# Optimization experiments

Hardware: AMD Instinct MI355X
Metric: run time of the kernel (lower is better)

Reference implementation:

```python
import jax, jax.numpy as jnp
import numpy as np

N_NODES = 8192
N_EDGES = 131072

_DIMS = [
    ("cnn1", 3, 32), ("cnn2", 32, 64), ("cnn3", 64, 128),
    ("gcn1", 128, 256), ("gcn2", 256, 512), ("gcn3", 512, 1024),
    ("cnnd1", 1024, 512), ("cnnd2", 512, 256), ("cnnd3", 256, 128), ("cnnd4", 128, 50),
]


def setup_inputs() -> dict:
    key = jax.random.key(0)
    ks = jax.random.split(key, 2 + 2 * len(_DIMS))
    inp = {
        "x": jax.random.normal(ks[0], (N_NODES, 3), dtype=jnp.float32),
        "edge_index": jax.random.randint(ks[1], (2, N_EDGES), 0, N_NODES, dtype=jnp.int64)
        if jax.config.jax_enable_x64 else
        jax.random.randint(ks[1], (2, N_EDGES), 0, N_NODES, dtype=jnp.int32),
    }
    for i, (name, din, dout) in enumerate(_DIMS):
        scale = 1.0 / np.sqrt(din)
        inp[name + "_w"] = jax.random.normal(ks[2 + 2 * i], (din, dout), dtype=jnp.float32) * scale
        inp[name + "_b"] = jax.random.normal(ks[3 + 2 * i], (dout,), dtype=jnp.float32) * scale
    return inp


def _gcn_norm(edge_index, n, dtype):
    # add self-loops, symmetric normalization D^{-1/2}(A+I)D^{-1/2}
    loop = jnp.arange(n, dtype=edge_index.dtype)
    src = jnp.concatenate([edge_index[0], loop])
    dst = jnp.concatenate([edge_index[1], loop])
    deg = jax.ops.segment_sum(jnp.ones_like(dst, dtype=dtype), dst, num_segments=n)
    dinv = jnp.where(deg > 0, 1.0 / jnp.sqrt(deg), 0.0)
    norm = dinv[src] * dinv[dst]  # [E+N]
    return src, dst, norm


def _forward(x, edge_index,
             cnn1_w, cnn1_b, cnn2_w, cnn2_b, cnn3_w, cnn3_b,
             gcn1_w, gcn1_b, gcn2_w, gcn2_b, gcn3_w, gcn3_b,
             cnnd1_w, cnnd1_b, cnnd2_w, cnnd2_b, cnnd3_w, cnnd3_b, cnnd4_w, cnnd4_b):
    n = x.shape[0]
    src, dst, norm = _gcn_norm(edge_index, n, x.dtype)

    def lin(h, w, b):  # 1x1 Conv1d == per-node linear
        return h @ w + b

    def gcn(h, w, b):
        hl = h @ w                                    # [N, out]
        msg = hl[src] * norm[:, None]                 # gather + scale [E+N, out]
        return jax.ops.segment_sum(msg, dst, num_segments=n) + b

    h = jax.nn.relu(lin(x, cnn1_w, cnn1_b))
    h = jax.nn.relu(lin(h, cnn2_w, cnn2_b))
    h = jax.nn.relu(lin(h, cnn3_w, cnn3_b))
    h = jax.nn.relu(gcn(h, gcn1_w, gcn1_b))
    h = jax.nn.relu(gcn(h, gcn2_w, gcn2_b))
    h = jax.nn.relu(gcn(h, gcn3_w, gcn3_b))
    h = jax.nn.relu(lin(h, cnnd1_w, cnnd1_b))
    h = jax.nn.relu(lin(h, cnnd2_w, cnnd2_b))
    h = jax.nn.relu(lin(h, cnnd3_w, cnnd3_b))
    h = lin(h, cnnd4_w, cnnd4_b)
    return jax.nn.softmax(h, axis=1)  # [N, output_dim]


def reference(x, edge_index,
              cnn1_w, cnn1_b, cnn2_w, cnn2_b, cnn3_w, cnn3_b,
              gcn1_w, gcn1_b, gcn2_w, gcn2_b, gcn3_w, gcn3_b,
              cnnd1_w, cnnd1_b, cnnd2_w, cnnd2_b, cnnd3_w, cnnd3_b, cnnd4_w, cnnd4_b):
    return _forward(x, edge_index,
                    cnn1_w, cnn1_b, cnn2_w, cnn2_b, cnn3_w, cnn3_b,
                    gcn1_w, gcn1_b, gcn2_w, gcn2_b, gcn3_w, gcn3_b,
                    cnnd1_w, cnnd1_b, cnnd2_w, cnnd2_b, cnnd3_w, cnnd3_b, cnnd4_w, cnnd4_b)
```

## Files before the change

### kernel.cpp

```cpp
#include <hip/hip_runtime.h>
#include <math.h>

#define N_NODES 8192
#define N_EDGES 131072

typedef unsigned short u16;
typedef unsigned int u32;
typedef short bf16x8 __attribute__((ext_vector_type(8)));
typedef int v4i __attribute__((ext_vector_type(4)));
typedef float f32x4 __attribute__((ext_vector_type(4)));

__device__ __forceinline__ u16 f2bf(float x) {
    unsigned u = __float_as_uint(x);
    u += 0x7fffu + ((u >> 16) & 1u);
    return (u16)(u >> 16);
}
__device__ __forceinline__ float bf2f(u16 h) { return __uint_as_float(((unsigned)h) << 16); }

#define GLD_LDS(gp, lp) __builtin_amdgcn_global_load_lds( \
    (const __attribute__((address_space(1))) void*)(gp),  \
    (__attribute__((address_space(3))) void*)(lp), 16, 0, 0)

template <int N> __device__ __forceinline__ void wait_vmcnt() {
    if constexpr (N == 0) asm volatile("s_waitcnt vmcnt(0)" ::: "memory");
    else if constexpr (N == 4) asm volatile("s_waitcnt vmcnt(4)" ::: "memory");
    else if constexpr (N == 8) asm volatile("s_waitcnt vmcnt(8)" ::: "memory");
    else static_assert(N < 0, "unsupported vmcnt");
}

__device__ __forceinline__ u32 lds_addr(const void* p) {
    return (u32)(size_t)(const __attribute__((address_space(3))) void*)p;
}

__device__ __forceinline__ bf16x8 lds_read_b128(u32 addr) {
    v4i r;
    asm volatile("ds_read_b128 %0, %1" : "=v"(r) : "v"(addr));
    union { v4i i; bf16x8 b; } u;
    u.i = r;
    return u.b;
}

template <int NU> struct UV;
template <> struct UV<1> { typedef u32 T; };
template <> struct UV<2> { typedef uint2 T; };
template <> struct UV<4> { typedef uint4 T; };


__global__ void k_zero_deg(int* __restrict__ deg) {
    int i = blockIdx.x * 256 + threadIdx.x;
    if (i < N_NODES) deg[i] = 0;
}

__global__ void k_count(const int* __restrict__ ei, int* __restrict__ deg) {
    int e = blockIdx.x * 256 + threadIdx.x;
    if (e < N_EDGES) atomicAdd(&deg[ei[N_EDGES + e]], 1);
}

__global__ __launch_bounds__(1024) void k_scan(const int* __restrict__ deg,
                                               int* __restrict__ rowptr,
                                               int* __restrict__ pos,
                                               float* __restrict__ dinv) {
    __shared__ int sums[1024];
    int t = threadIdx.x;
    int local[8];
    int s = 0;
#pragma unroll
    for (int i = 0; i < 8; ++i) {
        local[i] = deg[t * 8 + i];
        dinv[t * 8 + i] = 1.0f / sqrtf((float)(local[i] + 1));
        s += local[i];
    }
    sums[t] = s;
    __syncthreads();
    for (int off = 1; off < 1024; off <<= 1) {
        int v = (t >= off) ? sums[t - off] : 0;
        __syncthreads();
        sums[t] += v;
        __syncthreads();
    }
    int run = sums[t] - s;
#pragma unroll
    for (int i = 0; i < 8; ++i) {
        rowptr[t * 8 + i] = run;
        pos[t * 8 + i] = run;
        run += local[i];
    }
    if (t == 1023) rowptr[8192] = run;
}

__global__ void k_fill(const int* __restrict__ ei, const float* __restrict__ dinv,
                       int* __restrict__ pos, int* __restrict__ csr_src,
                       float* __restrict__ csr_w) {
    int e = blockIdx.x * 256 + threadIdx.x;
    if (e < N_EDGES) {
        int s = ei[e];
        int t = ei[N_EDGES + e];
        int idx = atomicAdd(&pos[t], 1);
        csr_src[idx] = s;
        csr_w[idx] = dinv[s] * dinv[t];
    }
}

__global__ void k_prep_all(const float* __restrict__ g1w, const float* __restrict__ g2w,
                           const float* __restrict__ g3w, const float* __restrict__ d1w,
                           const float* __restrict__ d2w, const float* __restrict__ d3w,
                           u16* __restrict__ wts) {
    int idx = blockIdx.x * 256 + threadIdx.x;
    const float* W;
    int local, lgK, N;
    u16 *hi, *lo;
    if (idx < 32768)        { W = g1w; local = idx;           lgK = 7;  N = 256;  hi = wts;           lo = wts + 32768; }
    else if (idx < 163840)  { W = g2w; local = idx - 32768;   lgK = 8;  N = 512;  hi = wts + 65536;   lo = wts + 196608; }
    else if (idx < 688128)  { W = g3w; local = idx - 163840;  lgK = 9;  N = 1024; hi = wts + 327680;  lo = wts + 851968; }
    else if (idx < 1212416) { W = d1w; local = idx - 688128;  lgK = 10; N = 512;  hi = wts + 1376256; lo = wts + 1900544; }
    else if (idx < 1343488) { W = d2w; local = idx - 1212416; lgK = 9;  N = 256;  hi = wts + 2424832; lo = wts + 2555904; }
    else if (idx < 1376256) { W = d3w; local = idx - 1343488; lgK = 8;  N = 128;  hi = wts + 2686976; lo = wts + 2719744; }
    else return;
    int n = local >> lgK;
    int k = local & ((1 << lgK) - 1);
    float v = W[(size_t)k * N + n];
    u16 h = f2bf(v);
    int dst = ((k >> 3) * N + n) * 8 + (k & 7);
    hi[dst] = h;
    lo[dst] = f2bf(v - bf2f(h));
}

__global__ __launch_bounds__(256) void k_enc_fused(const float* __restrict__ x,
                                                   const float* __restrict__ w1, const float* __restrict__ b1,
                                                   const float* __restrict__ w2, const float* __restrict__ b2,
                                                   const float* __restrict__ w3, const float* __restrict__ b3,
                                                   u16* __restrict__ Chi, u16* __restrict__ Clo) {
    __shared__ float lw[10560];
    const int tid = threadIdx.x;
    for (int i = tid; i < 96; i += 256) lw[i] = w1[i];
    for (int i = tid; i < 32; i += 256) lw[96 + i] = b1[i];
    for (int i = tid; i < 2048; i += 256) lw[128 + i] = w2[i];
    for (int i = tid; i < 64; i += 256) lw[2176 + i] = b2[i];
    for (int i = tid; i < 8192; i += 256) lw[2240 + i] = w3[i];
    for (int i = tid; i < 128; i += 256) lw[10432 + i] = b3[i];
    __syncthreads();

    const int lane = tid & 63;
    const int node = blockIdx.x * 4 + (tid >> 6);

    float x0 = x[node * 3 + 0], x1 = x[node * 3 + 1], x2 = x[node * 3 + 2];

    int o1 = lane & 31;
    float h1 = fmaxf(x0 * lw[o1] + x1 * lw[32 + o1] + x2 * lw[64 + o1] + lw[96 + o1], 0.f);

    float h2 = lw[2176 + lane];
#pragma unroll
    for (int k = 0; k < 32; ++k) h2 += __shfl(h1, k) * lw[128 + k * 64 + lane];
    h2 = fmaxf(h2, 0.f);

    float h3a = lw[10432 + lane];
    float h3b = lw[10432 + 64 + lane];
#pragma unroll
    for (int k = 0; k < 64; ++k) {
        float hk = __shfl(h2, k);
        h3a += hk * lw[2240 + k * 128 + lane];
        h3b += hk * lw[2240 + k * 128 + 64 + lane];
    }
    h3a = fmaxf(h3a, 0.f);
    h3b = fmaxf(h3b, 0.f);

    size_t base = (size_t)node * 128;
    u16 ha = f2bf(h3a), hb = f2bf(h3b);
    Chi[base + lane] = ha;
    Chi[base + 64 + lane] = hb;
    Clo[base + lane] = f2bf(h3a - bf2f(ha));
    Clo[base + 64 + lane] = f2bf(h3b - bf2f(hb));
}

__global__ __launch_bounds__(256) void k_d4sm_fused(const float* __restrict__ A,
                                                    const float* __restrict__ W,
                                                    const float* __restrict__ bias,
                                                    float* __restrict__ out) {
    __shared__ float lw[6450];
    const int tid = threadIdx.x;
    for (int i = tid; i < 6400; i += 256) lw[i] = W[i];
    for (int i = tid; i < 50; i += 256) lw[6400 + i] = bias[i];
    __syncthreads();

    const int lane = tid & 63;
    const int node = blockIdx.x * 4 + (tid >> 6);

    float a0 = A[(size_t)node * 128 + lane];
    float a1 = A[(size_t)node * 128 + 64 + lane];

    float acc = (lane < 50) ? lw[6400 + lane] : 0.f;
    int oc = (lane < 50) ? lane : 0;
#pragma unroll
    for (int k = 0; k < 64; ++k) acc += __shfl(a0, k) * lw[k * 50 + oc];
#pragma unroll
    for (int k = 0; k < 64; ++k) acc += __shfl(a1, k) * lw[(64 + k) * 50 + oc];

    float v = (lane < 50) ? acc : -INFINITY;
    float m = v;
#pragma unroll
    for (int off = 32; off; off >>= 1) m = fmaxf(m, __shfl_xor(m, off));
    float e = (lane < 50) ? expf(v - m) : 0.f;
    float s = e;
#pragma unroll
    for (int off = 32; off; off >>= 1) s += __shfl_xor(s, off);
    if (lane < 50) out[(size_t)node * 50 + lane] = e / s;
}

template <int D>
__global__ __launch_bounds__(256) void k_agg_s(const u16* __restrict__ hi_in,
                                               const u16* __restrict__ lo_in,
                                               u16* __restrict__ hi_out,
                                               u16* __restrict__ lo_out,
                                               const int* __restrict__ rowptr,
                                               const int* __restrict__ csr_src,
                                               const float* __restrict__ csr_w,
                                               const float* __restrict__ dinv) {
    constexpr int EPL = D / 64;
    constexpr int NU = EPL / 2;
    using VT = typename UV<NU>::T;
    int node = blockIdx.x * 4 + (threadIdx.x >> 6);
    int lane = threadIdx.x & 63;
    const size_t off = (size_t)node * D + lane * EPL;
    float acc[EPL];
    {
        float dn = dinv[node];
        float w0 = dn * dn;
        u32 hu[NU], lu[NU];
        *(VT*)hu = *(const VT*)(hi_in + off);
        *(VT*)lu = *(const VT*)(lo_in + off);
#pragma unroll
        for (int j = 0; j < NU; ++j) {
            acc[2 * j]     = (__uint_as_float(hu[j] << 16) + __uint_as_float(lu[j] << 16)) * w0;
            acc[2 * j + 1] = (__uint_as_float(hu[j] & 0xffff0000u) + __uint_as_float(lu[j] & 0xffff0000u)) * w0;
        }
    }
#define EDGE_ACC(S, W) do {                                                            \
        size_t so = (size_t)(S) * D + lane * EPL;                                      \
        u32 hu[NU], lu[NU];                                                            \
        *(VT*)hu = *(const VT*)(hi_in + so);                                           \
        *(VT*)lu = *(const VT*)(lo_in + so);                                           \
        _Pragma("unroll")                                                              \
        for (int j = 0; j < NU; ++j) {                                                 \
            acc[2 * j]     += (__uint_as_float(hu[j] << 16) + __uint_as_float(lu[j] << 16)) * (W); \
            acc[2 * j + 1] += (__uint_as_float(hu[j] & 0xffff0000u) + __uint_as_float(lu[j] & 0xffff0000u)) * (W); \
        }                                                                              \
    } while (0)
    int beg = rowptr[node], end = rowptr[node + 1];
    int e = beg;
    for (; e + 2 <= end; e += 2) {
        int s0 = csr_src[e], s1 = csr_src[e + 1];
        float wa = csr_w[e], wb = csr_w[e + 1];
        EDGE_ACC(s0, wa);
        EDGE_ACC(s1, wb);
    }
    if (e < end) EDGE_ACC(csr_src[e], csr_w[e]);
#undef EDGE_ACC
    u32 how[NU], low[NU];
#pragma unroll
    for (int j = 0; j < NU; ++j) {
        u16 h0 = f2bf(acc[2 * j]);     u16 l0 = f2bf(acc[2 * j] - bf2f(h0));
        u16 h1 = f2bf(acc[2 * j + 1]); u16 l1 = f2bf(acc[2 * j + 1] - bf2f(h1));
        how[j] = (u32)h0 | ((u32)h1 << 16);
        low[j] = (u32)l0 | ((u32)l1 << 16);
    }
    *(VT*)(hi_out + off) = *(VT*)how;
    *(VT*)(lo_out + off) = *(VT*)low;
}

template <int D>
__global__ __launch_bounds__(256) void k_agg(const float* __restrict__ h, float* __restrict__ out,
                                             const int* __restrict__ rowptr,
                                             const int* __restrict__ csr_src,
                                             const float* __restrict__ csr_w,
                                             const float* __restrict__ dinv) {
    constexpr int NF2 = D / 128;
    int node = blockIdx.x * 4 + (threadIdx.x >> 6);
    int lane = threadIdx.x & 63;
    const float2* hn = (const float2*)(h + (size_t)node * D);
    float dn = dinv[node];
    float w0 = dn * dn;
    float2 acc[NF2];
#pragma unroll
    for (int j = 0; j < NF2; ++j) {
        float2 v = hn[lane + j * 64];
        acc[j].x = v.x * w0;
        acc[j].y = v.y * w0;
    }
    int beg = rowptr[node], end = rowptr[node + 1];
    for (int e = beg; e < end; ++e) {
        int s = csr_src[e];
        float w = csr_w[e];
        const float2* hs = (const float2*)(h + (size_t)s * D);
#pragma unroll
        for (int j = 0; j < NF2; ++j) {
            float2 v = hs[lane + j * 64];
            acc[j].x += v.x * w;
            acc[j].y += v.y * w;
        }
    }
    float2* op = (float2*)(out + (size_t)node * D);
#pragma unroll
    for (int j = 0; j < NF2; ++j) op[lane + j * 64] = acc[j];
}

template <int OUTS>
__global__ __launch_bounds__(64) void k_linear_small(const float* __restrict__ A,
                                                     const float* __restrict__ W,
                                                     const float* __restrict__ bias,
                                                     float* __restrict__ Cf,
                                                     u16* __restrict__ Chi,
                                                     u16* __restrict__ Clo,
                                                     int K, int N, int relu) {
    int n = blockIdx.y;
    int o = blockIdx.x * 64 + threadIdx.x;
    if (o >= N) return;
    float s = bias[o];
    const float* a = A + (size_t)n * K;
    for (int k = 0; k < K; ++k) s += a[k] * W[(size_t)k * N + o];
    if (relu) s = fmaxf(s, 0.0f);
    if (OUTS == 0) {
        Cf[(size_t)n * N + o] = s;
    } else {
        u16 h = f2bf(s);
        Chi[(size_t)n * N + o] = h;
        Clo[(size_t)n * N + o] = f2bf(s - bf2f(h));
    }
}

template <int OUTS>
__global__ __launch_bounds__(256, 2) void k_gemm_mfma(
    const u16* __restrict__ Ahi, const u16* __restrict__ Alo,
    const u16* __restrict__ Bhi, const u16* __restrict__ Blo,
    const float* __restrict__ bias,
    float* __restrict__ Cf, u16* __restrict__ Chi, u16* __restrict__ Clo,
    int M, int N, int K, int relu) {
    constexpr int BM = 128, BN = 128, WN = 32;
    constexpr int BK = 32;
    constexpr int FM = BM / 16, FN = WN / 16;
    constexpr int ASZ = (BK / 8) * BM * 16;
    constexpr int TOT = 2 * ASZ;
    constexpr int NSTG = TOT / 4096;

    __shared__ char lds0[TOT] __attribute__((aligned(16)));
    __shared__ char lds1[TOT] __attribute__((aligned(16)));

    const int tid = threadIdx.x;
    const int lane = tid & 63;
    const int wave = tid >> 6;

    const int nwg = gridDim.x * gridDim.y;
    const int d = blockIdx.y * gridDim.x + blockIdx.x;
    const int q = nwg >> 3;
    const int lg = (d & 7) * q + (d >> 3);
    const int bx = lg % gridDim.x, by = lg / gridDim.x;
    const int m0 = by * BM, n0 = bx * BN;

    const u16* gp[NSTG];
    int ldo[NSTG];
#pragma unroll
    for (int i = 0; i < NSTG; ++i) {
        int o = i * 4096 + tid * 16;
        ldo[i] = o;
        const u16* base;
        int roff;
        if (o < ASZ) { base = Ahi; roff = o; }
        else         { base = Alo; roff = o - ASZ; }
        int c = roff / (BM * 16);
        int r = (roff % (BM * 16)) / 16;
        gp[i] = base + (size_t)(m0 + r) * K + c * 8;
    }

    const int kc = lane >> 4, rr = lane & 15;
    const int aoff = (kc * BM + rr) * 16;

    const size_t bbase = ((size_t)kc * N + n0 + wave * WN + rr) * 8;
    const size_t bstep = (size_t)4 * N * 8;

    f32x4 acc[FM][FN];
#pragma unroll
    for (int i = 0; i < FM; ++i)
#pragma unroll
        for (int j = 0; j < FN; ++j) acc[i][j] = f32x4{0.f, 0.f, 0.f, 0.f};

    bf16x8 b0h[FN], b0l[FN], b1h[FN], b1l[FN];

#define STAGE(P, KS) do {                                          \
        _Pragma("unroll")                                          \
        for (int i = 0; i < NSTG; ++i)                             \
            GLD_LDS(gp[i] + (KS) * BK, (P) + ldo[i]);              \
    } while (0)

#define LOADB(BH, BL, KS) do {                                                      \
        _Pragma("unroll")                                                           \
        for (int fn = 0; fn < FN; ++fn) {                                           \
            BH[fn] = *(const bf16x8*)(Bhi + bbase + (size_t)(KS) * bstep + fn * 128); \
            BL[fn] = *(const bf16x8*)(Blo + bbase + (size_t)(KS) * bstep + fn * 128); \
        }                                                                           \
    } while (0)

#define STEP(CUR, DST, BHC, BLC, BHD, BLD, KS) do {                                 \
        if ((KS) + 1 < nks) LOADB(BHD, BLD, (KS) + 1);                              \
        __builtin_amdgcn_sched_barrier(0);                                          \
        if ((KS) + 1 < nks) wait_vmcnt<4>(); else wait_vmcnt<0>();                  \
        asm volatile("s_barrier" ::: "memory");                                     \
        if ((KS) + 1 < nks) STAGE(DST, (KS) + 1);                                   \
        const u32 pb_ = lds_addr(CUR);                                              \
        bf16x8 ah[FM], al[FM];                                                      \
        _Pragma("unroll")                                                           \
        for (int fm = 0; fm < FM; ++fm) {                                           \
            ah[fm] = lds_read_b128(pb_ + aoff + fm * 256);                          \
            al[fm] = lds_read_b128(pb_ + ASZ + aoff + fm * 256);                    \
        }                                                                           \
        asm volatile("s_waitcnt lgkmcnt(0)");                                       \
        __builtin_amdgcn_sched_barrier(0);                                          \
        __builtin_amdgcn_s_setprio(1);                                              \
        _Pragma("unroll")                                                           \
        for (int fm = 0; fm < FM; ++fm)                                             \
            _Pragma("unroll")                                                       \
            for (int fn = 0; fn < FN; ++fn) {                                       \
                acc[fm][fn] = __builtin_amdgcn_mfma_f32_16x16x32_bf16(ah[fm], BHC[fn], acc[fm][fn], 0, 0, 0); \
                acc[fm][fn] = __builtin_amdgcn_mfma_f32_16x16x32_bf16(al[fm], BHC[fn], acc[fm][fn], 0, 0, 0); \
                acc[fm][fn] = __builtin_amdgcn_mfma_f32_16x16x32_bf16(ah[fm], BLC[fn], acc[fm][fn], 0, 0, 0); \
            }                                                                       \
        __builtin_amdgcn_s_setprio(0);                                              \
    } while (0)

    const int nks = K / BK;
    LOADB(b0h, b0l, 0);
    STAGE(lds0, 0);
    for (int base = 0; base < nks; base += 2) {
        STEP(lds0, lds1, b0h, b0l, b1h, b1l, base);
        STEP(lds1, lds0, b1h, b1l, b0h, b0l, base + 1);
    }
    asm volatile("" ::: "memory");
#undef STEP
#undef LOADB
#undef STAGE

    const int cr = (lane >> 4) * 4;
    const int cc = lane & 15;
#pragma unroll
    for (int fm = 0; fm < FM; ++fm)
#pragma unroll
        for (int fn = 0; fn < FN; ++fn) {
            int col = n0 + wave * WN + fn * 16 + cc;
            float bv = bias[col];
#pragma unroll
            for (int r = 0; r < 4; ++r) {
                int row = m0 + fm * 16 + cr + r;
                float v = acc[fm][fn][r] + bv;
                if (relu) v = fmaxf(v, 0.f);
                if (OUTS == 0) {
                    Cf[(size_t)row * N + col] = v;
                } else {
                    u16 h = f2bf(v);
                    Chi[(size_t)row * N + col] = h;
                    Clo[(size_t)row * N + col] = f2bf(v - bf2f(h));
                }
            }
        }
}

template <int BM, int BN, int BK, int TM, int TN>
__global__ __launch_bounds__(256) void k_gemm(const float* __restrict__ A,
                                              const float* __restrict__ W,
                                              const float* __restrict__ bias,
                                              float* __restrict__ C,
                                              int M, int N, int K, int relu) {
    constexpr int TX = BN / TN;
    constexpr int TY = BM / TM;
    __shared__ float As[BK][BM + 4];
    __shared__ float Bs[BK][BN];
    int tid = threadIdx.x;
    int tx = tid % TX, ty = tid / TX;
    int m0 = blockIdx.y * BM, n0 = blockIdx.x * BN;
    float acc[TM][TN] = {};
    for (int k0 = 0; k0 < K; k0 += BK) {
        for (int v = tid; v < BM * BK / 4; v += TX * TY) {
            int r = v / (BK / 4);
            int kcp = (v % (BK / 4)) * 4;
            float4 val = *(const float4*)&A[(size_t)(m0 + r) * K + k0 + kcp];
            As[kcp + 0][r] = val.x; As[kcp + 1][r] = val.y;
            As[kcp + 2][r] = val.z; As[kcp + 3][r] = val.w;
        }
        for (int v = tid; v < BK * BN / 4; v += TX * TY) {
            int kr = v / (BN / 4);
            int c = (v % (BN / 4)) * 4;
            *(float4*)&Bs[kr][c] = *(const float4*)&W[(size_t)(k0 + kr) * N + n0 + c];
        }
        __syncthreads();
#pragma unroll
        for (int kk = 0; kk < BK; ++kk) {
            float a[TM], b[TN];
#pragma unroll
            for (int i = 0; i < TM; i += 4) {
                float4 t4 = *(const float4*)&As[kk][ty * TM + i];
                a[i] = t4.x; a[i + 1] = t4.y; a[i + 2] = t4.z; a[i + 3] = t4.w;
            }
#pragma unroll
            for (int j = 0; j < TN; j += 4) {
                float4 t4 = *(const float4*)&Bs[kk][tx * TN + j];
                b[j] = t4.x; b[j + 1] = t4.y; b[j + 2] = t4.z; b[j + 3] = t4.w;
            }
#pragma unroll
            for (int i = 0; i < TM; ++i)
#pragma unroll
                for (int j = 0; j < TN; ++j) acc[i][j] += a[i] * b[j];
        }
        __syncthreads();
    }
#pragma unroll
    for (int i = 0; i < TM; ++i) {
        int row = m0 + ty * TM + i;
#pragma unroll
        for (int j = 0; j < TN; j += 4) {
            int col = n0 + tx * TN + j;
            float4 v;
            v.x = acc[i][j + 0] + bias[col + 0];
            v.y = acc[i][j + 1] + bias[col + 1];
            v.z = acc[i][j + 2] + bias[col + 2];
            v.w = acc[i][j + 3] + bias[col + 3];
            if (relu) {
                v.x = fmaxf(v.x, 0.0f); v.y = fmaxf(v.y, 0.0f);
                v.z = fmaxf(v.z, 0.0f); v.w = fmaxf(v.w, 0.0f);
            }
            *(float4*)&C[(size_t)row * N + col] = v;
        }
    }
}

__global__ __launch_bounds__(256) void k_softmax50(const float* __restrict__ in,
                                                   float* __restrict__ out) {
    int row = blockIdx.x * 4 + (threadIdx.x >> 6);
    int lane = threadIdx.x & 63;
    float v = (lane < 50) ? in[(size_t)row * 50 + lane] : -INFINITY;
    float m = v;
#pragma unroll
    for (int off = 32; off; off >>= 1) m = fmaxf(m, __shfl_xor(m, off));
    float e = (lane < 50) ? expf(v - m) : 0.0f;
    float s = e;
#pragma unroll
    for (int off = 32; off; off >>= 1) s += __shfl_xor(s, off);
    if (lane < 50) out[(size_t)row * 50 + lane] = e / s;
}


extern "C" void kernel_launch(void* const* d_in, const int* in_sizes, int n_in,
                              void* d_out, int out_size, void* d_ws, size_t ws_size,
                              hipStream_t stream) {
    const float* x  = (const float*)d_in[0];
    const int*   ei = (const int*)d_in[1];
    const float *w1  = (const float*)d_in[2],  *b1  = (const float*)d_in[3];
    const float *w2  = (const float*)d_in[4],  *b2  = (const float*)d_in[5];
    const float *w3  = (const float*)d_in[6],  *b3  = (const float*)d_in[7];
    const float *g1w = (const float*)d_in[8],  *g1b = (const float*)d_in[9];
    const float *g2w = (const float*)d_in[10], *g2b = (const float*)d_in[11];
    const float *g3w = (const float*)d_in[12], *g3b = (const float*)d_in[13];
    const float *d1w = (const float*)d_in[14], *d1b = (const float*)d_in[15];
    const float *d2w = (const float*)d_in[16], *d2b = (const float*)d_in[17];
    const float *d3w = (const float*)d_in[18], *d3b = (const float*)d_in[19];
    const float *d4w = (const float*)d_in[20], *d4b = (const float*)d_in[21];
    float* out = (float*)d_out;

    const size_t NEED_NEW = 57016576ull;

    if (ws_size >= NEED_NEW) {
        char* w = (char*)d_ws;
        u16* p0hi = (u16*)w;
        u16* p0lo = (u16*)(w + 16777216);
        u16* p1hi = (u16*)(w + 33554432);
        u16* p1lo = (u16*)(w + 41943040);
        float* f0 = (float*)p1hi;
        u16* wts = (u16*)(w + 50331648);
        u16 *wt1h = wts,            *wt1l = wt1h + 32768;
        u16 *wt2h = wt1l + 32768,   *wt2l = wt2h + 131072;
        u16 *wt3h = wt2l + 131072,  *wt3l = wt3h + 524288;
        u16 *wd1h = wt3l + 524288,  *wd1l = wd1h + 524288;
        u16 *wd2h = wd1l + 524288,  *wd2l = wd2h + 131072;
        u16 *wd3h = wd2l + 131072,  *wd3l = wd3h + 32768;
        char* cs = w + 55836672;
        int*   deg     = (int*)cs;
        int*   rowptr  = deg + N_NODES;
        int*   pos     = rowptr + 8256;
        float* dinv    = (float*)(pos + N_NODES);
        int*   csr_src = (int*)(dinv + N_NODES);
        float* csr_w   = (float*)(csr_src + N_EDGES);

        k_zero_deg<<<N_NODES / 256, 256, 0, stream>>>(deg);
        k_count<<<N_EDGES / 256, 256, 0, stream>>>(ei, deg);
        k_scan<<<1, 1024, 0, stream>>>(deg, rowptr, pos, dinv);
        k_fill<<<N_EDGES / 256, 256, 0, stream>>>(ei, dinv, pos, csr_src, csr_w);

        k_prep_all<<<1376256 / 256, 256, 0, stream>>>(g1w, g2w, g3w, d1w, d2w, d3w, wts);

        k_enc_fused<<<N_NODES / 4, 256, 0, stream>>>(x, w1, b1, w2, b2, w3, b3, p0hi, p0lo);

        k_agg_s<128><<<N_NODES / 4, 256, 0, stream>>>(p0hi, p0lo, p1hi, p1lo, rowptr, csr_src, csr_w, dinv);
        k_gemm_mfma<1><<<dim3(256 / 128, N_NODES / 128), 256, 0, stream>>>(
            p1hi, p1lo, wt1h, wt1l, g1b, nullptr, p0hi, p0lo, N_NODES, 256, 128, 1);
        k_agg_s<256><<<N_NODES / 4, 256, 0, stream>>>(p0hi, p0lo, p1hi, p1lo, rowptr, csr_src, csr_w, dinv);
        k_gemm_mfma<1><<<dim3(512 / 128, N_NODES / 128), 256, 0, stream>>>(
            p1hi, p1lo, wt2h, wt2l, g2b, nullptr, p0hi, p0lo, N_NODES, 512, 256, 1);
        k_agg_s<512><<<N_NODES / 4, 256, 0, stream>>>(p0hi, p0lo, p1hi, p1lo, rowptr, csr_src, csr_w, dinv);
        k_gemm_mfma<1><<<dim3(1024 / 128, N_NODES / 128), 256, 0, stream>>>(
            p1hi, p1lo, wt3h, wt3l, g3b, nullptr, p0hi, p0lo, N_NODES, 1024, 512, 1);
        k_gemm_mfma<1><<<dim3(512 / 128, N_NODES / 128), 256, 0, stream>>>(
            p0hi, p0lo, wd1h, wd1l, d1b, nullptr, p1hi, p1lo, N_NODES, 512, 1024, 1);
        k_gemm_mfma<1><<<dim3(256 / 128, N_NODES / 128), 256, 0, stream>>>(
            p1hi, p1lo, wd2h, wd2l, d2b, nullptr, p0hi, p0lo, N_NODES, 256, 512, 1);
        k_gemm_mfma<0><<<dim3(128 / 128, N_NODES / 128), 256, 0, stream>>>(
            p0hi, p0lo, wd3h, wd3l, d3b, f0, nullptr, nullptr, N_NODES, 128, 256, 1);

        k_d4sm_fused<<<N_NODES / 4, 256, 0, stream>>>(f0, d4w, d4b, out);
    } else {
        float* bufA = (float*)d_ws;
        float* bufB = bufA + (size_t)N_NODES * 1024;
        int*   deg     = (int*)(bufB + (size_t)N_NODES * 512);
        int*   rowptr  = deg + N_NODES;
        int*   pos     = rowptr + 8256;
        float* dinv    = (float*)(pos + N_NODES);
        int*   csr_src = (int*)(dinv + N_NODES);
        float* csr_w   = (float*)(csr_src + N_EDGES);

        k_zero_deg<<<N_NODES / 256, 256, 0, stream>>>(deg);
        k_count<<<N_EDGES / 256, 256, 0, stream>>>(ei, deg);
        k_scan<<<1, 1024, 0, stream>>>(deg, rowptr, pos, dinv);
        k_fill<<<N_EDGES / 256, 256, 0, stream>>>(ei, dinv, pos, csr_src, csr_w);

        k_linear_small<0><<<dim3(1, N_NODES), 64, 0, stream>>>(x,    w1, b1, bufA, nullptr, nullptr, 3, 32, 1);
        k_linear_small<0><<<dim3(1, N_NODES), 64, 0, stream>>>(bufA, w2, b2, bufB, nullptr, nullptr, 32, 64, 1);
        k_linear_small<0><<<dim3(2, N_NODES), 64, 0, stream>>>(bufB, w3, b3, bufA, nullptr, nullptr, 64, 128, 1);

        k_agg<128><<<N_NODES / 4, 256, 0, stream>>>(bufA, bufB, rowptr, csr_src, csr_w, dinv);
        k_gemm<64, 64, 16, 4, 4><<<dim3(256 / 64, N_NODES / 64), 256, 0, stream>>>(
            bufB, g1w, g1b, bufA, N_NODES, 256, 128, 1);
        k_agg<256><<<N_NODES / 4, 256, 0, stream>>>(bufA, bufB, rowptr, csr_src, csr_w, dinv);
        k_gemm<128, 128, 16, 8, 8><<<dim3(512 / 128, N_NODES / 128), 256, 0, stream>>>(
            bufB, g2w, g2b, bufA, N_NODES, 512, 256, 1);
        k_agg<512><<<N_NODES / 4, 256, 0, stream>>>(bufA, bufB, rowptr, csr_src, csr_w, dinv);
        k_gemm<128, 128, 16, 8, 8><<<dim3(1024 / 128, N_NODES / 128), 256, 0, stream>>>(
            bufB, g3w, g3b, bufA, N_NODES, 1024, 512, 1);
        k_gemm<128, 128, 16, 8, 8><<<dim3(512 / 128, N_NODES / 128), 256, 0, stream>>>(
            bufA, d1w, d1b, bufB, N_NODES, 512, 1024, 1);
        k_gemm<64, 64, 16, 4, 4><<<dim3(256 / 64, N_NODES / 64), 256, 0, stream>>>(
            bufB, d2w, d2b, bufA, N_NODES, 256, 512, 1);
        k_gemm<64, 64, 16, 4, 4><<<dim3(128 / 64, N_NODES / 64), 256, 0, stream>>>(
            bufA, d3w, d3b, bufB, N_NODES, 128, 256, 1);
        k_linear_small<0><<<dim3(1, N_NODES), 64, 0, stream>>>(bufB, d4w, d4b, bufA, nullptr, nullptr, 128, 50, 0);
        k_softmax50<<<N_NODES / 4, 256, 0, stream>>>(bufA, out);
    }
}
```

Baseline: 285.5 us.

## Add 128x256-tile triple-buffered MFMA GEMM with XCD-aware block remapping

Adds a new split-bf16 GEMM kernel that uses 512 threads and a 128x256 output tile. It stages A and B hi/lo fragments into three rotating LDS buffers, waiting on vmcnt(6), and remaps block indices so neighbouring tiles land on the same XCD. Five of the six dense GEMMs now use it, which raises per-block data reuse and pipelining depth. The cost is half as many workgroups per layer, leaving the smaller layers with few blocks for the CUs, and roughly 144KB of LDS per block. The vmcnt(8) helper variant is replaced with vmcnt(6).

```diff
diff --git a/kernel.cpp b/kernel.cpp
--- a/kernel.cpp
+++ b/kernel.cpp
@@ -24,7 +24,7 @@
 template <int N> __device__ __forceinline__ void wait_vmcnt() {
     if constexpr (N == 0) asm volatile("s_waitcnt vmcnt(0)" ::: "memory");
     else if constexpr (N == 4) asm volatile("s_waitcnt vmcnt(4)" ::: "memory");
-    else if constexpr (N == 8) asm volatile("s_waitcnt vmcnt(8)" ::: "memory");
+    else if constexpr (N == 6) asm volatile("s_waitcnt vmcnt(6)" ::: "memory");
     else static_assert(N < 0, "unsupported vmcnt");
 }
 
@@ -325,6 +325,144 @@
         Chi[(size_t)n * N + o] = h;
         Clo[(size_t)n * N + o] = f2bf(s - bf2f(h));
     }
+}
+
+template <int OUTS>
+__global__ __launch_bounds__(512, 1) void k_gemm_mfma2(
+    const u16* __restrict__ Ahi, const u16* __restrict__ Alo,
+    const u16* __restrict__ Bhi, const u16* __restrict__ Blo,
+    const float* __restrict__ bias,
+    float* __restrict__ Cf, u16* __restrict__ Chi, u16* __restrict__ Clo,
+    int M, int N, int K, int relu) {
+    constexpr int BM = 128, BN = 256, BK = 32;
+    constexpr int FM = 4, FN = 4;
+    constexpr int ASZ = 4 * BM * 16;
+    constexpr int BSZ = 4 * BN * 16;
+    constexpr int TOT = 2 * ASZ + 2 * BSZ;
+    constexpr int NLD = TOT / (512 * 16);
+
+    __shared__ char lds0[TOT] __attribute__((aligned(16)));
+    __shared__ char lds1[TOT] __attribute__((aligned(16)));
+    __shared__ char lds2[TOT] __attribute__((aligned(16)));
+
+    const int tid = threadIdx.x;
+    const int lane = tid & 63;
+    const int wave = tid >> 6;
+    const int wy = wave >> 2;
+    const int wx = wave & 3;
+
+    const int nwg = gridDim.x * gridDim.y;
+    const int d = blockIdx.y * gridDim.x + blockIdx.x;
+    const int q = nwg >> 3;
+    const int lg = (d & 7) * q + (d >> 3);
+    const int bx = lg % gridDim.x, by = lg / gridDim.x;
+    const int m0 = by * BM, n0 = bx * BN;
+
+    const u16* gp[NLD];
+    size_t st[NLD];
+    int ldo[NLD];
+#pragma unroll
+    for (int i = 0; i < NLD; ++i) {
+        int o = i * 8192 + tid * 16;
+        ldo[i] = o;
+        if (o < 2 * ASZ) {
+            const u16* base = (o < ASZ) ? Ahi : Alo;
+            int roff = (o < ASZ) ? o : o - ASZ;
+            int c = roff / (BM * 16);
+            int r = (roff % (BM * 16)) / 16;
+            gp[i] = base + (size_t)(m0 + r) * K + c * 8;
+            st[i] = BK;
+        } else {
+            int bo = o - 2 * ASZ;
+            const u16* base = (bo < BSZ) ? Bhi : Blo;
+            int roff = (bo < BSZ) ? bo : bo - BSZ;
+            int c = roff / (BN * 16);
+            int n = (roff % (BN * 16)) / 16;
+            gp[i] = base + ((size_t)c * N + n0 + n) * 8;
+            st[i] = (size_t)32 * N;
+        }
+    }
+
+    const int kc = lane >> 4, rr = lane & 15;
+    const int aoff = (kc * BM + wy * 64 + rr) * 16;
+    const int boff = 2 * ASZ + (kc * BN + wx * 64 + rr) * 16;
+
+    f32x4 acc[FM][FN];
+#pragma unroll
+    for (int i = 0; i < FM; ++i)
+#pragma unroll
+        for (int j = 0; j < FN; ++j) acc[i][j] = f32x4{0.f, 0.f, 0.f, 0.f};
+
+#define STAGE2(P, KS) do {                                         \
+        _Pragma("unroll")                                          \
+        for (int i = 0; i < NLD; ++i)                              \
+            GLD_LDS(gp[i] + (size_t)(KS) * st[i], (P) + ldo[i]);   \
+    } while (0)
+
+#define STEP2(CUR, DST, KS) do {                                                    \
+        if ((KS) + 1 < nks) wait_vmcnt<6>(); else wait_vmcnt<0>();                  \
+        asm volatile("s_barrier" ::: "memory");                                     \
+        if ((KS) + 2 < nks) STAGE2(DST, (KS) + 2);                                  \
+        const u32 pb_ = lds_addr(CUR);                                              \
+        bf16x8 ah[FM], al[FM], bh[FN], bl[FN];                                      \
+        _Pragma("unroll")                                                           \
+        for (int fm = 0; fm < FM; ++fm) {                                           \
+            ah[fm] = lds_read_b128(pb_ + aoff + fm * 256);                          \
+            al[fm] = lds_read_b128(pb_ + ASZ + aoff + fm * 256);                    \
+        }                                                                           \
+        _Pragma("unroll")                                                           \
+        for (int fn = 0; fn < FN; ++fn) {                                           \
+            bh[fn] = lds_read_b128(pb_ + boff + fn * 256);                          \
+            bl[fn] = lds_read_b128(pb_ + BSZ + boff + fn * 256);                    \
+        }                                                                           \
+        asm volatile("s_waitcnt lgkmcnt(0)");                                       \
+        __builtin_amdgcn_sched_barrier(0);                                          \
+        __builtin_amdgcn_s_setprio(1);                                              \
+        _Pragma("unroll")                                                           \
+        for (int fm = 0; fm < FM; ++fm)                                             \
+            _Pragma("unroll")                                                       \
+            for (int fn = 0; fn < FN; ++fn) {                                       \
+                acc[fm][fn] = __builtin_amdgcn_mfma_f32_16x16x32_bf16(ah[fm], bh[fn], acc[fm][fn], 0, 0, 0); \
+                acc[fm][fn] = __builtin_amdgcn_mfma_f32_16x16x32_bf16(al[fm], bh[fn], acc[fm][fn], 0, 0, 0); \
+                acc[fm][fn] = __builtin_amdgcn_mfma_f32_16x16x32_bf16(ah[fm], bl[fn], acc[fm][fn], 0, 0, 0); \
+            }                                                                       \
+        __builtin_amdgcn_s_setprio(0);                                              \
+    } while (0)
+
+    const int nks = K / BK;
+    STAGE2(lds0, 0);
+    STAGE2(lds1, 1);
+    for (int base = 0; base < nks; base += 3) {
+        STEP2(lds0, lds2, base);
+        if (base + 1 < nks) STEP2(lds1, lds0, base + 1);
+        if (base + 2 < nks) STEP2(lds2, lds1, base + 2);
+    }
+    asm volatile("" ::: "memory");
+#undef STEP2
+#undef STAGE2
+
+    const int cr = (lane >> 4) * 4;
+    const int cc = lane & 15;
+#pragma unroll
+    for (int fm = 0; fm < FM; ++fm)
+#pragma unroll
+        for (int fn = 0; fn < FN; ++fn) {
+            int col = n0 + wx * 64 + fn * 16 + cc;
+            float bv = bias[col];
+#pragma unroll
+            for (int r = 0; r < 4; ++r) {
+                int row = m0 + wy * 64 + fm * 16 + cr + r;
+                float v = acc[fm][fn][r] + bv;
+                if (relu) v = fmaxf(v, 0.f);
+                if (OUTS == 0) {
+                    Cf[(size_t)row * N + col] = v;
+                } else {
+                    u16 h = f2bf(v);
+                    Chi[(size_t)row * N + col] = h;
+                    Clo[(size_t)row * N + col] = f2bf(v - bf2f(h));
+                }
+            }
+        }
 }
 
 template <int OUTS>
@@ -596,19 +734,19 @@
         k_enc_fused<<<N_NODES / 4, 256, 0, stream>>>(x, w1, b1, w2, b2, w3, b3, p0hi, p0lo);
 
         k_agg_s<128><<<N_NODES / 4, 256, 0, stream>>>(p0hi, p0lo, p1hi, p1lo, rowptr, csr_src, csr_w, dinv);
-        k_gemm_mfma<1><<<dim3(256 / 128, N_NODES / 128), 256, 0, stream>>>(
+        k_gemm_mfma2<1><<<dim3(1, N_NODES / 128), 512, 0, stream>>>(
             p1hi, p1lo, wt1h, wt1l, g1b, nullptr, p0hi, p0lo, N_NODES, 256, 128, 1);
         k_agg_s<256><<<N_NODES / 4, 256, 0, stream>>>(p0hi, p0lo, p1hi, p1lo, rowptr, csr_src, csr_w, dinv);
-        k_gemm_mfma<1><<<dim3(512 / 128, N_NODES / 128), 256, 0, stream>>>(
+        k_gemm_mfma2<1><<<dim3(2, N_NODES / 128), 512, 0, stream>>>(
             p1hi, p1lo, wt2h, wt2l, g2b, nullptr, p0hi, p0lo, N_NODES, 512, 256, 1);
         k_agg_s<512><<<N_NODES / 4, 256, 0, stream>>>(p0hi, p0lo, p1hi, p1lo, rowptr, csr_src, csr_w, dinv);
-        k_gemm_mfma<1><<<dim3(1024 / 128, N_NODES / 128), 256, 0, stream>>>(
+        k_gemm_mfma2<1><<<dim3(4, N_NODES / 128), 512, 0, stream>>>(
             p1hi, p1lo, wt3h, wt3l, g3b, nullptr, p0hi, p0lo, N_NODES, 1024, 512, 1);
-        k_gemm_mfma<1><<<dim3(512 / 128, N_NODES / 128), 256, 0, stream>>>(
+        k_gemm_mfma2<1><<<dim3(2, N_NODES / 128), 512, 0, stream>>>(
             p0hi, p0lo, wd1h, wd1l, d1b, nullptr, p1hi, p1lo, N_NODES, 512, 1024, 1);
-        k_gemm_mfma<1><<<dim3(256 / 128, N_NODES / 128), 256, 0, stream>>>(
+        k_gemm_mfma2<1><<<dim3(1, N_NODES / 128), 512, 0, stream>>>(
             p1hi, p1lo, wd2h, wd2l, d2b, nullptr, p0hi, p0lo, N_NODES, 256, 512, 1);
-        k_gemm_mfma<0><<<dim3(128 / 128, N_NODES / 128), 256, 0, stream>>>(
+        k_gemm_mfma<0><<<dim3(1, N_NODES / 128), 256, 0, stream>>>(
             p0hi, p0lo, wd3h, wd3l, d3b, f0, nullptr, nullptr, N_NODES, 128, 256, 1);
 
         k_d4sm_fused<<<N_NODES / 4, 256, 0, stream>>>(f0, d4w, d4b, out);
```

Result: slower. 305.4 us (+7.0%).
